# Kernel optimization log

Hardware: AMD Instinct MI355X
Metric: run time of the kernel (lower is better)

The kernel has to match this reference:

```python
import jax, jax.numpy as jnp
import numpy as np

N = 50000   # full-order mesh size
n = 10      # latent dim
MU = 32     # neighbourhood / window size
B = 8       # batch of snapshots


def setup_inputs() -> dict:
    key = jax.random.key(0)
    ks = jax.random.split(key, 6)
    x = jax.random.normal(ks[0], (B, N), jnp.float32)
    enc_w = jax.random.normal(ks[1], (n, N), jnp.float32) * 0.01  # torch Linear weight [n, N]
    enc_b = jax.random.normal(ks[2], (n,), jnp.float32) * 0.01
    decoder = jax.random.uniform(ks[3], (n, N), jnp.float32, minval=-0.01, maxval=0.01)
    bandwidth_layers = jax.random.uniform(ks[4], (n, n, N), jnp.float32, minval=-0.01, maxval=0.01)
    neighbours = jax.random.randint(ks[5], (N, MU), 0, N, jnp.int32)
    return dict(x=x, enc_w=enc_w, enc_b=enc_b, decoder=decoder,
                bandwidth_layers=bandwidth_layers, neighbours=neighbours)


def reference(x, enc_w, enc_b, decoder, bandwidth_layers, neighbours):
    mu = neighbours.shape[1]
    # encode: torch Linear -> x @ W.T + b                      [B, n]
    encoded = x @ enc_w.T + enc_b
    # bandwidths: bmm(encoded.repeat(n,1,1), bw).permute(1,0,2) -> sigmoid   [B, n, N]
    w = jax.nn.sigmoid(jnp.einsum('bk,ikp->bip', encoded, bandwidth_layers))
    # bubble window per scalar w: relu(1 - x^2/(w*mu)^2), normalized over mu  [B, n, N, mu]
    xs2 = (jnp.arange(mu, dtype=x.dtype) ** 2)  # [mu]
    win = jax.nn.relu(1.0 - xs2 / (w[..., None] * mu) ** 2)
    win = win / jnp.sum(win, axis=-1, keepdims=True)
    # gather decoder rows at each node's neighbours            [n, N, mu]
    gathered = jnp.take(decoder, neighbours, axis=1)
    # smooth_vec: sum over neighbourhood                       [B, n, N]
    smoothed = jnp.einsum('ipm,bipm->bip', gathered, win)
    # final bmm: encoded [B,1,n] @ smoothed [B,n,N] -> [B,N]
    return jnp.einsum('bi,bip->bp', encoded, smoothed)
```

## Files before the change

### kernel.cpp

```cpp
#include <hip/hip_runtime.h>
#include <hip/hip_bf16.h>

#define N_NODES 50000
#define NLAT 10
#define MU 32
#define BATCH 8
#define CHUNK 2000
#define NCHUNK 25
#define ENC_BLOCKS (BATCH * NLAT * NCHUNK)
#define TR_BLOCKS ((N_NODES + 255) / 256)
#define DT_STRIDE 16
#define NPB 64

typedef float v2f __attribute__((ext_vector_type(2)));

static __device__ __forceinline__ v2f v2_fma(v2f a, v2f b, v2f c) {
#if __has_builtin(__builtin_elementwise_fma)
    return __builtin_elementwise_fma(a, b, c);
#else
    v2f r; r[0] = fmaf(a[0], b[0], c[0]); r[1] = fmaf(a[1], b[1], c[1]); return r;
#endif
}
static __device__ __forceinline__ v2f v2_max0(v2f a) {
#if __has_builtin(__builtin_elementwise_max)
    v2f z = {0.0f, 0.0f};
    return __builtin_elementwise_max(a, z);
#else
    v2f r; r[0] = fmaxf(a[0], 0.0f); r[1] = fmaxf(a[1], 0.0f); return r;
#endif
}

__global__ __launch_bounds__(256) void encode_a_transpose(
    const float* __restrict__ x, const float* __restrict__ enc_w,
    const float* __restrict__ dec,
    float* __restrict__ partial, float* __restrict__ dec_t) {
    const int bid = blockIdx.x;
    if (bid < ENC_BLOCKS) {
        const int c  = bid % NCHUNK;
        const int bi = bid / NCHUNK;
        const int b = bi / NLAT, i = bi % NLAT;
        const float4* xr = (const float4*)(x + (size_t)b * N_NODES + c * CHUNK);
        const float4* wr = (const float4*)(enc_w + (size_t)i * N_NODES + c * CHUNK);
        float part = 0.0f;
        for (int q = threadIdx.x; q < CHUNK / 4; q += 256) {
            float4 xv = xr[q], wv = wr[q];
            part += xv.x * wv.x + xv.y * wv.y + xv.z * wv.z + xv.w * wv.w;
        }
        for (int off = 32; off; off >>= 1) part += __shfl_down(part, off, 64);
        __shared__ float s[4];
        if ((threadIdx.x & 63) == 0) s[threadIdx.x >> 6] = part;
        __syncthreads();
        if (threadIdx.x == 0) partial[bid] = (s[0] + s[1]) + (s[2] + s[3]);
    } else {
        const int p = (bid - ENC_BLOCKS) * 256 + threadIdx.x;
        if (p >= N_NODES) return;
        float v[DT_STRIDE];
        #pragma unroll
        for (int i = 0; i < NLAT; ++i) v[i] = dec[(size_t)i * N_NODES + p];
        #pragma unroll
        for (int i = NLAT; i < DT_STRIDE; ++i) v[i] = 0.0f;
        float4* dst = (float4*)(dec_t + (size_t)p * DT_STRIDE);
        #pragma unroll
        for (int q = 0; q < 4; ++q)
            dst[q] = make_float4(v[4*q], v[4*q+1], v[4*q+2], v[4*q+3]);
    }
}

__global__ __launch_bounds__(320) void nrbs_main_kernel(
    const float* __restrict__ dec_t,
    const float* __restrict__ bw,
    const int*   __restrict__ nbr,
    const float* __restrict__ partial,
    const float* __restrict__ enc_b,
    float*       __restrict__ out) {
    __shared__ float s_enc[BATCH * NLAT];
    __shared__ float s_inv[NLAT][4][NPB][2];
    __shared__ int   s_nbr[NPB][MU + 1];
    __shared__ int   s_tm[NPB];
    __shared__ float s_red[NLAT][BATCH][NPB];
    const int tid   = threadIdx.x;
    const int node0 = blockIdx.x * NPB;

    if (tid < BATCH * NLAT) {
        float s = 0.0f;
        #pragma unroll
        for (int c = 0; c < NCHUNK; ++c) s += partial[tid * NCHUNK + c];
        s_enc[tid] = s + enc_b[tid % NLAT];
    }
    if (tid < NPB) s_tm[tid] = 0;
    for (int j = tid; j < NPB * MU / 4; j += 320) {
        const int node = j >> 3, ch = j & 7;
        int4 v = make_int4(0, 0, 0, 0);
        if (node0 + node < N_NODES)
            v = ((const int4*)(nbr + (size_t)(node0 + node) * MU))[ch];
        s_nbr[node][ch * 4 + 0] = v.x; s_nbr[node][ch * 4 + 1] = v.y;
        s_nbr[node][ch * 4 + 2] = v.z; s_nbr[node][ch * 4 + 3] = v.w;
    }
    __syncthreads();

    const int g  = tid >> 6;
    const int nl = tid & 63;
    const int i0 = 2 * g;
    const int p  = node0 + nl;
    const bool act = (p < N_NODES);

    if (act) {
        float tloc = 0.0f;
        #pragma unroll
        for (int ii = 0; ii < 2; ++ii) {
            const int i = i0 + ii;
            float bwv[NLAT];
            #pragma unroll
            for (int k = 0; k < NLAT; ++k)
                bwv[k] = bw[((size_t)(i * NLAT + k)) * N_NODES + p];
            #pragma unroll
            for (int b = 0; b < BATCH; ++b) {
                float z = 0.0f;
                #pragma unroll
                for (int k = 0; k < NLAT; ++k)
                    z = fmaf(s_enc[b * NLAT + k], bwv[k], z);
                const float w = 1.0f / (1.0f + __expf(-z));
                const float t = w * (float)MU;
                tloc = fmaxf(tloc, t);
                s_inv[i][b >> 1][nl][b & 1] = __builtin_amdgcn_rcpf(t * t);
            }
        }
        atomicMax(&s_tm[nl], __float_as_int(tloc));
    }
    __syncthreads();

    if (act) {
        v2f inv2[2][4], asum[2][4], ssum[2][4];
        #pragma unroll
        for (int ii = 0; ii < 2; ++ii)
            #pragma unroll
            for (int b2 = 0; b2 < 4; ++b2) {
                inv2[ii][b2] = *(const v2f*)&s_inv[i0 + ii][b2][nl][0];
                asum[ii][b2] = (v2f){0.0f, 0.0f};
                ssum[ii][b2] = (v2f){0.0f, 0.0f};
            }
        const int mcap = min(MU, (int)__int_as_float(s_tm[nl]) + 1);

        for (int m = 0; m < mcap; ++m) {
            const int idx = s_nbr[nl][m];
            const v2f g2 = *(const v2f*)(dec_t + (size_t)idx * DT_STRIDE + i0);
            const float m2 = (float)(m * m);
            const v2f nm2 = {-m2, -m2}, one = {1.0f, 1.0f};
            #pragma unroll
            for (int ii = 0; ii < 2; ++ii) {
                const v2f gb = {g2[ii], g2[ii]};
                #pragma unroll
                for (int b2 = 0; b2 < 4; ++b2) {
                    v2f win = v2_max0(v2_fma(nm2, inv2[ii][b2], one));
                    ssum[ii][b2] += win;
                    asum[ii][b2] = v2_fma(gb, win, asum[ii][b2]);
                }
            }
        }
        #pragma unroll
        for (int ii = 0; ii < 2; ++ii)
            #pragma unroll
            for (int b2 = 0; b2 < 4; ++b2)
                #pragma unroll
                for (int h = 0; h < 2; ++h) {
                    const int b = b2 * 2 + h;
                    s_red[i0 + ii][b][nl] =
                        s_enc[b * NLAT + i0 + ii] * asum[ii][b2][h] *
                        __builtin_amdgcn_rcpf(ssum[ii][b2][h]);
                }
    }
    __syncthreads();

    if (tid < 256) {
        const int b = tid >> 5, q = tid & 31;
        #pragma unroll
        for (int h = 0; h < 2; ++h) {
            const int node = q + 32 * h, p2 = node0 + node;
            if (p2 < N_NODES) {
                float s = 0.0f;
                #pragma unroll
                for (int i = 0; i < NLAT; ++i) s += s_red[i][b][node];
                out[(size_t)b * N_NODES + p2] = s;
            }
        }
    }
}

extern "C" void kernel_launch(void* const* d_in, const int* in_sizes, int n_in,
                              void* d_out, int out_size, void* d_ws, size_t ws_size,
                              hipStream_t stream) {
    const float* x       = (const float*)d_in[0];
    const float* enc_w   = (const float*)d_in[1];
    const float* enc_b   = (const float*)d_in[2];
    const float* decoder = (const float*)d_in[3];
    const float* bwl     = (const float*)d_in[4];
    const int*   nbr     = (const int*)d_in[5];
    float* out = (float*)d_out;

    float* partial = (float*)((char*)d_ws + 1024);
    float* dec_t   = (float*)((char*)d_ws + 65536);

    encode_a_transpose<<<ENC_BLOCKS + TR_BLOCKS, 256, 0, stream>>>(
        x, enc_w, decoder, partial, dec_t);

    const int blocks = (N_NODES + NPB - 1) / NPB;
    nrbs_main_kernel<<<blocks, 320, 0, stream>>>(
        dec_t, bwl, nbr, partial, enc_b, out);
}
```

Measured before the change: 121.5 us.

## Remap main kernel to one thread per node-latent pair with shuffle reduction

```diff
diff --git a/kernel.cpp b/kernel.cpp
--- a/kernel.cpp
+++ b/kernel.cpp
@@ -10,7 +10,7 @@
 #define ENC_BLOCKS (BATCH * NLAT * NCHUNK)
 #define TR_BLOCKS ((N_NODES + 255) / 256)
 #define DT_STRIDE 16
-#define NPB 64
+#define NPB 32
 
 typedef float v2f __attribute__((ext_vector_type(2)));
 
@@ -66,7 +66,7 @@
     }
 }
 
-__global__ __launch_bounds__(320) void nrbs_main_kernel(
+__global__ __launch_bounds__(512) void nrbs_main_kernel(
     const float* __restrict__ dec_t,
     const float* __restrict__ bw,
     const int*   __restrict__ nbr,
@@ -74,10 +74,9 @@
     const float* __restrict__ enc_b,
     float*       __restrict__ out) {
     __shared__ float s_enc[BATCH * NLAT];
-    __shared__ float s_inv[NLAT][4][NPB][2];
+    __shared__ float s_inv[NLAT][NPB][BATCH];
+    __shared__ float s_tm[NLAT][NPB];
     __shared__ int   s_nbr[NPB][MU + 1];
-    __shared__ int   s_tm[NPB];
-    __shared__ float s_red[NLAT][BATCH][NPB];
     const int tid   = threadIdx.x;
     const int node0 = blockIdx.x * NPB;
 
@@ -87,102 +86,106 @@
         for (int c = 0; c < NCHUNK; ++c) s += partial[tid * NCHUNK + c];
         s_enc[tid] = s + enc_b[tid % NLAT];
     }
-    if (tid < NPB) s_tm[tid] = 0;
-    for (int j = tid; j < NPB * MU / 4; j += 320) {
-        const int node = j >> 3, ch = j & 7;
-        int4 v = make_int4(0, 0, 0, 0);
-        if (node0 + node < N_NODES)
-            v = ((const int4*)(nbr + (size_t)(node0 + node) * MU))[ch];
-        s_nbr[node][ch * 4 + 0] = v.x; s_nbr[node][ch * 4 + 1] = v.y;
-        s_nbr[node][ch * 4 + 2] = v.z; s_nbr[node][ch * 4 + 3] = v.w;
+    {
+        const int j = tid;
+        if (j < NPB * MU / 4) {
+            const int node = j >> 3, ch = j & 7;
+            int4 v = make_int4(0, 0, 0, 0);
+            if (node0 + node < N_NODES)
+                v = ((const int4*)(nbr + (size_t)(node0 + node) * MU))[ch];
+            s_nbr[node][ch * 4 + 0] = v.x; s_nbr[node][ch * 4 + 1] = v.y;
+            s_nbr[node][ch * 4 + 2] = v.z; s_nbr[node][ch * 4 + 3] = v.w;
+        }
     }
     __syncthreads();
 
-    const int g  = tid >> 6;
-    const int nl = tid & 63;
-    const int i0 = 2 * g;
-    const int p  = node0 + nl;
-    const bool act = (p < N_NODES);
-
-    if (act) {
-        float tloc = 0.0f;
-        #pragma unroll
-        for (int ii = 0; ii < 2; ++ii) {
-            const int i = i0 + ii;
+    {
+        const int w    = tid >> 6;
+        const int lane = tid & 63;
+        const int half = lane >> 5;
+        const int node = lane & 31;
+        const int i    = w + 8 * half;
+        const int p    = node0 + node;
+        if (i < NLAT && p < N_NODES) {
             float bwv[NLAT];
             #pragma unroll
             for (int k = 0; k < NLAT; ++k)
                 bwv[k] = bw[((size_t)(i * NLAT + k)) * N_NODES + p];
+            float tloc = 0.0f;
+            float invv[BATCH];
             #pragma unroll
             for (int b = 0; b < BATCH; ++b) {
                 float z = 0.0f;
                 #pragma unroll
                 for (int k = 0; k < NLAT; ++k)
                     z = fmaf(s_enc[b * NLAT + k], bwv[k], z);
-                const float w = 1.0f / (1.0f + __expf(-z));
-                const float t = w * (float)MU;
+                const float sg = 1.0f / (1.0f + __expf(-z));
+                const float t  = sg * (float)MU;
                 tloc = fmaxf(tloc, t);
-                s_inv[i][b >> 1][nl][b & 1] = __builtin_amdgcn_rcpf(t * t);
+                invv[b] = __builtin_amdgcn_rcpf(t * t);
             }
-        }
-        atomicMax(&s_tm[nl], __float_as_int(tloc));
+            float4* dst = (float4*)&s_inv[i][node][0];
+            dst[0] = make_float4(invv[0], invv[1], invv[2], invv[3]);
+            dst[1] = make_float4(invv[4], invv[5], invv[6], invv[7]);
+            s_tm[i][node] = tloc;
+        }
     }
     __syncthreads();
 
+    const int node  = tid >> 4;
+    const int islot = tid & 15;
+    const int p     = node0 + node;
+    const bool act  = (islot < NLAT) && (p < N_NODES);
+
+    v2f inv2[4], asum[4], ssum[4];
+    #pragma unroll
+    for (int b2 = 0; b2 < 4; ++b2) {
+        inv2[b2] = (v2f){0.0f, 0.0f};
+        asum[b2] = (v2f){0.0f, 0.0f};
+        ssum[b2] = (v2f){0.0f, 0.0f};
+    }
+    int mcap = 0;
     if (act) {
-        v2f inv2[2][4], asum[2][4], ssum[2][4];
-        #pragma unroll
-        for (int ii = 0; ii < 2; ++ii)
-            #pragma unroll
-            for (int b2 = 0; b2 < 4; ++b2) {
-                inv2[ii][b2] = *(const v2f*)&s_inv[i0 + ii][b2][nl][0];
-                asum[ii][b2] = (v2f){0.0f, 0.0f};
-                ssum[ii][b2] = (v2f){0.0f, 0.0f};
-            }
-        const int mcap = min(MU, (int)__int_as_float(s_tm[nl]) + 1);
-
-        for (int m = 0; m < mcap; ++m) {
-            const int idx = s_nbr[nl][m];
-            const v2f g2 = *(const v2f*)(dec_t + (size_t)idx * DT_STRIDE + i0);
-            const float m2 = (float)(m * m);
-            const v2f nm2 = {-m2, -m2}, one = {1.0f, 1.0f};
-            #pragma unroll
-            for (int ii = 0; ii < 2; ++ii) {
-                const v2f gb = {g2[ii], g2[ii]};
-                #pragma unroll
-                for (int b2 = 0; b2 < 4; ++b2) {
-                    v2f win = v2_max0(v2_fma(nm2, inv2[ii][b2], one));
-                    ssum[ii][b2] += win;
-                    asum[ii][b2] = v2_fma(gb, win, asum[ii][b2]);
-                }
-            }
-        }
-        #pragma unroll
-        for (int ii = 0; ii < 2; ++ii)
-            #pragma unroll
-            for (int b2 = 0; b2 < 4; ++b2)
-                #pragma unroll
-                for (int h = 0; h < 2; ++h) {
-                    const int b = b2 * 2 + h;
-                    s_red[i0 + ii][b][nl] =
-                        s_enc[b * NLAT + i0 + ii] * asum[ii][b2][h] *
-                        __builtin_amdgcn_rcpf(ssum[ii][b2][h]);
-                }
-    }
-    __syncthreads();
-
-    if (tid < 256) {
-        const int b = tid >> 5, q = tid & 31;
+        const float4* iv = (const float4*)&s_inv[islot][node][0];
+        const float4 a = iv[0], c = iv[1];
+        inv2[0] = (v2f){a.x, a.y}; inv2[1] = (v2f){a.z, a.w};
+        inv2[2] = (v2f){c.x, c.y}; inv2[3] = (v2f){c.z, c.w};
+        mcap = min(MU, (int)s_tm[islot][node] + 1);
+    }
+
+    for (int m = 0; m < mcap; ++m) {
+        const int idx = s_nbr[node][m];
+        const float g = dec_t[(size_t)idx * DT_STRIDE + islot];
+        const float m2 = (float)(m * m);
+        const v2f nm2 = {-m2, -m2}, one = {1.0f, 1.0f}, gg = {g, g};
+        #pragma unroll
+        for (int b2 = 0; b2 < 4; ++b2) {
+            const v2f win = v2_max0(v2_fma(nm2, inv2[b2], one));
+            ssum[b2] += win;
+            asum[b2] = v2_fma(gg, win, asum[b2]);
+        }
+    }
+
+    float r[BATCH];
+    #pragma unroll
+    for (int b2 = 0; b2 < 4; ++b2)
         #pragma unroll
         for (int h = 0; h < 2; ++h) {
-            const int node = q + 32 * h, p2 = node0 + node;
-            if (p2 < N_NODES) {
-                float s = 0.0f;
-                #pragma unroll
-                for (int i = 0; i < NLAT; ++i) s += s_red[i][b][node];
-                out[(size_t)b * N_NODES + p2] = s;
-            }
-        }
+            const int b = 2 * b2 + h;
+            r[b] = act ? s_enc[b * NLAT + islot] * asum[b2][h] *
+                         __builtin_amdgcn_rcpf(ssum[b2][h])
+                       : 0.0f;
+        }
+    #pragma unroll
+    for (int mask = 1; mask < 16; mask <<= 1)
+        #pragma unroll
+        for (int b = 0; b < BATCH; ++b)
+            r[b] += __shfl_xor(r[b], mask, 16);
+
+    if (islot == 0 && p < N_NODES) {
+        #pragma unroll
+        for (int b = 0; b < BATCH; ++b)
+            out[(size_t)b * N_NODES + p] = r[b];
     }
 }
 
@@ -204,6 +207,6 @@
         x, enc_w, decoder, partial, dec_t);
 
     const int blocks = (N_NODES + NPB - 1) / NPB;
-    nrbs_main_kernel<<<blocks, 320, 0, stream>>>(
+    nrbs_main_kernel<<<blocks, 512, 0, stream>>>(
         dec_t, bwl, nbr, partial, enc_b, out);
 }
```

After: 107.6 us. -11.5%, faster.
